# Kernel optimization log

Hardware: AMD Instinct MI355X
Metric: run time of the kernel (lower is better)

Reference implementation:

```python
import jax, jax.numpy as jnp
import numpy as np

D_MODEL = 1024
NUM_HEAD = 16
D_K = D_MODEL // NUM_HEAD


def setup_inputs() -> dict:
    key = jax.random.key(0)
    ks = jax.random.split(key, 11)
    B, S = 2, 2048
    s = 1.0 / np.sqrt(D_MODEL)
    return {
        "q": jax.random.normal(ks[0], (B, S, D_MODEL), jnp.float32),
        "k": jax.random.normal(ks[1], (B, S, D_MODEL), jnp.float32),
        "v": jax.random.normal(ks[2], (B, S, D_MODEL), jnp.float32),
        "Wq": jax.random.normal(ks[3], (D_MODEL, D_MODEL), jnp.float32) * s,
        "bq": jnp.zeros((D_MODEL,), jnp.float32),
        "Wk": jax.random.normal(ks[4], (D_MODEL, D_MODEL), jnp.float32) * s,
        "bk": jnp.zeros((D_MODEL,), jnp.float32),
        "Wv": jax.random.normal(ks[5], (D_MODEL, D_MODEL), jnp.float32) * s,
        "bv": jnp.zeros((D_MODEL,), jnp.float32),
        "Wo": jax.random.normal(ks[6], (D_MODEL, D_MODEL), jnp.float32) * s,
        "bo": jnp.zeros((D_MODEL,), jnp.float32),
    }


def _split_head(x, B):
    # [B, S, d_model] -> [B, H, S, d_k]
    S = x.shape[1]
    return x.reshape(B, S, NUM_HEAD, D_K).transpose(0, 2, 1, 3)


def reference(q, k, v, Wq, bq, Wk, bk, Wv, bv, Wo, bo):
    B = q.shape[0]
    qh = _split_head(q @ Wq + bq, B)  # [B,H,Sq,dk]
    kh = _split_head(k @ Wk + bk, B)  # [B,H,Sk,dk]
    vh = _split_head(v @ Wv + bv, B)  # [B,H,Sk,dk]
    scores = jnp.einsum("bhqd,bhkd->bhqk", qh, kh) / jnp.sqrt(
        jnp.asarray(D_K, qh.dtype)
    )
    attn = jax.nn.softmax(scores, axis=-1)
    out = jnp.einsum("bhqk,bhkd->bhqd", attn, vh)  # [B,H,Sq,dk]
    out = out.transpose(0, 2, 1, 3).reshape(B, -1, D_MODEL)
    return jax.nn.relu(out @ Wo + bo)
```

## Files before the change

### kernel.cpp

```cpp
#include <hip/hip_runtime.h>
#include <math.h>

#define SEQ 2048
#define NHD 16

typedef float f32x4 __attribute__((ext_vector_type(4), may_alias));
typedef _Float16 h16x8 __attribute__((ext_vector_type(8), may_alias));
typedef _Float16 h16x4 __attribute__((ext_vector_type(4), may_alias));

__device__ __forceinline__ void gl_lds16(const void* g, void* l) {
  __builtin_amdgcn_global_load_lds(
      (const __attribute__((address_space(1))) unsigned int*)g,
      (__attribute__((address_space(3))) unsigned int*)l, 16, 0, 0);
}

struct PrepArgs {
  const float* W[4];
  _Float16* T[4];
  const float* X[3];
  _Float16* H[3];
};

__global__ __launch_bounds__(256) void prep_k(PrepArgs a) {
  __shared__ float tile[64][65];
  const int blk = blockIdx.x;
  const int t = threadIdx.x;
  if (blk < 1024) {
    const int widx = blk >> 8, tl = blk & 255;
    const int nb = (tl & 15) * 64, kb = (tl >> 4) * 64;
    const float* __restrict__ W = a.W[widx];
    _Float16* __restrict__ T = a.T[widx];
    const int c = t & 63, r0 = t >> 6;
#pragma unroll
    for (int i = 0; i < 16; ++i) {
      const int r = i * 4 + r0;
      tile[r][c] = W[(size_t)(kb + r) * 1024 + nb + c];
    }
    __syncthreads();
#pragma unroll
    for (int i = 0; i < 16; ++i) {
      const int n = i * 4 + r0;
      T[(size_t)(nb + n) * 1024 + kb + c] = (_Float16)tile[c][n];
    }
  } else {
    const int b2 = blk - 1024;
    const int z = b2 >> 11, bx = b2 & 2047;
    const float* __restrict__ X = a.X[z];
    _Float16* __restrict__ H = a.H[z];
    const size_t i = ((size_t)bx * 256 + t) * 8;
    const f32x4 f0 = *(const f32x4*)(X + i);
    const f32x4 f1 = *(const f32x4*)(X + i + 4);
    const float fs[8] = {f0.x, f0.y, f0.z, f0.w, f1.x, f1.y, f1.z, f1.w};
    h16x8 o;
#pragma unroll
    for (int j = 0; j < 8; ++j) o[j] = (_Float16)fs[j];
    *(h16x8*)(H + i) = o;
  }
}

struct QKVArgs {
  const _Float16* A[3];
  const _Float16* Bt[3];
  const float* bias[3];
  _Float16* C[3];
};

__global__ __launch_bounds__(512, 2) void gemm_qkv_k(QKVArgs a) {
  __shared__ __align__(16) char smem[131072];
  const int dblk = blockIdx.x;
  const int z = dblk >> 6;
  const int rb = dblk & 63;
  const int m0 = (rb >> 2) * 256;
  const int n0 = (rb & 3) * 256;
  const _Float16* __restrict__ A = a.A[z];
  const _Float16* __restrict__ Bt = a.Bt[z];
  const float* __restrict__ bias = a.bias[z];
  _Float16* __restrict__ C = a.C[z];

  const int t = threadIdx.x;
  const int l = t & 63, w = t >> 6;
  const int quad = l >> 4, l15 = l & 15;
  const int wm = w >> 2, wn = w & 3;

  const int srow = t >> 3;
  const int sslot = (t & 7) ^ (srow & 7);
  size_t goffA[4], goffB[4];
#pragma unroll
  for (int j = 0; j < 4; ++j) {
    goffA[j] = (size_t)(m0 + j * 64 + srow) * 1024 + sslot * 8;
    goffB[j] = (size_t)(n0 + j * 64 + srow) * 1024 + sslot * 8;
  }

  auto stage = [&](int buf, int kt) {
    const int k0 = kt * 64;
    char* base = smem + buf * 65536;
#pragma unroll
    for (int j = 0; j < 4; ++j) {
      gl_lds16(A + goffA[j] + k0, base + j * 8192 + w * 1024);
      gl_lds16(Bt + goffB[j] + k0, base + 32768 + j * 8192 + w * 1024);
    }
  };

  const f32x4 z4 = {0.f, 0.f, 0.f, 0.f};
  f32x4 acc[8][4];
#pragma unroll
  for (int i = 0; i < 8; ++i)
#pragma unroll
    for (int j = 0; j < 4; ++j) acc[i][j] = z4;

  const int xr = l15 & 7;

  stage(0, 0);
  for (int kt = 0; kt < 16; ++kt) {
    const int cur = kt & 1;
    if (kt < 15) {
      stage(cur ^ 1, kt + 1);
      asm volatile("s_waitcnt vmcnt(8)" ::: "memory");
    } else {
      asm volatile("s_waitcnt vmcnt(0)" ::: "memory");
    }
    __builtin_amdgcn_sched_barrier(0);
    __builtin_amdgcn_s_barrier();

    const char* base = smem + cur * 65536;
    h16x8 bf[4][2];
#pragma unroll
    for (int nj = 0; nj < 4; ++nj) {
      const int rowB = wn * 64 + nj * 16 + l15;
#pragma unroll
      for (int h = 0; h < 2; ++h) {
        const int sl = (h * 4 + quad) ^ xr;
        bf[nj][h] = *(const h16x8*)(base + 32768 + rowB * 128 + sl * 16);
      }
    }
#pragma unroll
    for (int mi = 0; mi < 8; ++mi) {
      const int rowA = wm * 128 + mi * 16 + l15;
      const h16x8 af0 = *(const h16x8*)(base + rowA * 128 + ((quad ^ xr) * 16));
      const h16x8 af1 = *(const h16x8*)(base + rowA * 128 + (((4 + quad) ^ xr) * 16));
#pragma unroll
      for (int nj = 0; nj < 4; ++nj) {
        acc[mi][nj] = __builtin_amdgcn_mfma_f32_16x16x32_f16(af0, bf[nj][0], acc[mi][nj], 0, 0, 0);
        acc[mi][nj] = __builtin_amdgcn_mfma_f32_16x16x32_f16(af1, bf[nj][1], acc[mi][nj], 0, 0, 0);
      }
    }
    __builtin_amdgcn_sched_barrier(0);
    __builtin_amdgcn_s_barrier();
  }

  if (z < 2) {
#pragma unroll
    for (int mi = 0; mi < 8; ++mi)
#pragma unroll
      for (int nj = 0; nj < 4; ++nj) {
        const int col = n0 + wn * 64 + nj * 16 + l15;
        const float bv = bias[col];
#pragma unroll
        for (int r = 0; r < 4; ++r) {
          const int row = m0 + wm * 128 + mi * 16 + quad * 4 + r;
          const int b = row >> 11, s = row & 2047;
          const int h = col >> 6, d = col & 63;
          C[((size_t)(b * NHD + h) * SEQ + s) * 64 + d] = (_Float16)(acc[mi][nj][r] + bv);
        }
      }
  } else {
    _Float16* sh = (_Float16*)smem;
#pragma unroll
    for (int mi = 0; mi < 8; ++mi)
#pragma unroll
      for (int nj = 0; nj < 4; ++nj) {
        const int col = wn * 64 + nj * 16 + l15;
        const float bv = bias[n0 + col];
#pragma unroll
        for (int r = 0; r < 4; ++r) {
          const int row = wm * 128 + mi * 16 + quad * 4 + r;
          sh[row * 256 + col] = (_Float16)(acc[mi][nj][r] + bv);
        }
      }
    __syncthreads();
    const int dr = t >> 1;
    const int half = t & 1;
    const int hh = dr >> 6, d = dr & 63;
    const int b = m0 >> 11, sbase = m0 & 2047;
    const int colL = hh * 64 + d;
    const size_t gbase =
        ((size_t)((b * NHD + (n0 >> 6) + hh) * 64 + d)) * SEQ + sbase + half * 128;
#pragma unroll
    for (int m8 = 0; m8 < 16; ++m8) {
      const int qq = half * 128 + m8 * 8;
      h16x8 ov;
#pragma unroll
      for (int j = 0; j < 8; ++j) {
        const int q = qq + j;
        const int g = q >> 6, p = q & 63;
        const int c = (p >> 2) + ((p & 3) << 4);
        ov[j] = sh[(g * 64 + c) * 256 + colL];
      }
      *(h16x8*)(C + gbase + m8 * 8) = ov;
    }
  }
}

__global__ __launch_bounds__(256) void gemm_o_k(
    const _Float16* __restrict__ Op0, const _Float16* __restrict__ Op1,
    const float* __restrict__ Lp, const _Float16* __restrict__ Bt,
    const float* __restrict__ bias, float* __restrict__ Cf) {
  __shared__ char smem[40960];
  float* inv_lds = (float*)(smem + 32768);
  const int rb = blockIdx.x;
  const int n0 = ((rb >> 3) & 7) * 128;
  const int m0 = ((((rb >> 6) << 3) | (rb & 7))) * 128;
  const int t = threadIdx.x;
  const int l = t & 63, w = t >> 6;
  const int quad = l >> 4, l15 = l & 15;
  const int wm = w >> 1, wn = w & 1;
  const int arow0 = t >> 2, aq = t & 3;

#pragma unroll
  for (int e = t; e < 2048; e += 256) {
    const int rl = e >> 4, hh = e & 15;
    const int m = m0 + rl;
    const int b = m >> 11, s = m & 2047;
    const size_t li = (size_t)(b * NHD + hh) * 2048 + s;
    inv_lds[e] = 1.f / (Lp[li] + Lp[65536 + li]);
  }
  __syncthreads();

  auto stageB = [&](int buf, int k0) {
#pragma unroll
    for (int it = 0; it < 2; ++it) {
      const int c = it * 4 + w;
      const int rr = c * 16 + l15;
      gl_lds16(Bt + (size_t)(n0 + rr) * 1024 + k0 + quad * 8,
               smem + buf * 8192 + c * 1024);
    }
  };
  auto loadA = [&](int k0, h16x8 (&r0)[2], h16x8 (&r1)[2]) {
#pragma unroll
    for (int it = 0; it < 2; ++it) {
      const size_t off = (size_t)(m0 + it * 64 + arow0) * 1024 + k0 + aq * 8;
      r0[it] = *(const h16x8*)(Op0 + off);
      r1[it] = *(const h16x8*)(Op1 + off);
    }
  };
  auto writeA = [&](int buf, int k0, const h16x8 (&r0)[2], const h16x8 (&r1)[2]) {
    const int head = k0 >> 6;
    h16x8* alds = (h16x8*)(smem + 16384 + buf * 8192);
#pragma unroll
    for (int it = 0; it < 2; ++it) {
      const int row = it * 64 + arow0;
      const int slot = (row >> 4) * 64 + aq * 16 + ((row & 15) ^ (aq * 2));
      const float inv = inv_lds[row * 16 + head];
      h16x8 hv;
#pragma unroll
      for (int j = 0; j < 8; ++j)
        hv[j] = (_Float16)(((float)r0[it][j] + (float)r1[it][j]) * inv);
      alds[slot] = hv;
    }
  };

  const f32x4 z4 = {0.f, 0.f, 0.f, 0.f};
  f32x4 acc[4][4];
#pragma unroll
  for (int i = 0; i < 4; ++i)
#pragma unroll
    for (int j = 0; j < 4; ++j) acc[i][j] = z4;

  h16x8 a0r[2], a1r[2];
  loadA(0, a0r, a1r);
  stageB(0, 0);
  writeA(0, 0, a0r, a1r);
  __syncthreads();
  int cur = 0;
  for (int k0 = 0; k0 < 1024; k0 += 32) {
    const int nk = k0 + 32;
    if (nk < 1024) {
      loadA(nk, a0r, a1r);
      stageB(cur ^ 1, nk);
    }
    const h16x8* blds = (const h16x8*)(smem + cur * 8192);
    const h16x8* alds = (const h16x8*)(smem + 16384 + cur * 8192);
    h16x8 af[4], bf[4];
#pragma unroll
    for (int i = 0; i < 4; ++i) {
      af[i] = alds[(wm * 4 + i) * 64 + quad * 16 + (l15 ^ (quad * 2))];
      bf[i] = blds[(wn * 4 + i) * 64 + l];
    }
#pragma unroll
    for (int i = 0; i < 4; ++i)
#pragma unroll
      for (int j = 0; j < 4; ++j)
        acc[i][j] = __builtin_amdgcn_mfma_f32_16x16x32_f16(af[i], bf[j], acc[i][j], 0, 0, 0);
    if (nk < 1024) writeA(cur ^ 1, nk, a0r, a1r);
    __syncthreads();
    cur ^= 1;
  }
#pragma unroll
  for (int i = 0; i < 4; ++i)
#pragma unroll
    for (int j = 0; j < 4; ++j) {
      const int col = n0 + wn * 64 + j * 16 + l15;
      const float bv = bias[col];
#pragma unroll
      for (int r = 0; r < 4; ++r) {
        const int row = m0 + wm * 64 + i * 16 + quad * 4 + r;
        Cf[(size_t)row * 1024 + col] = fmaxf(acc[i][j][r] + bv, 0.f);
      }
    }
}

__global__ __launch_bounds__(256, 4) void attn_k(
    const _Float16* __restrict__ Qf, const _Float16* __restrict__ Kf,
    const _Float16* __restrict__ Vtp,
    _Float16* __restrict__ Op0, _Float16* __restrict__ Op1,
    float* __restrict__ Lp) {
  __shared__ char smem[34816];
  h16x8* lds8 = (h16x8*)smem;
  const int dblk = blockIdx.x;
  const int comb = ((dblk >> 7) << 3) | (dblk & 7);
  const int q0 = ((dblk >> 3) & 15) * 128;
  const int bh = comb >> 1;
  const int kz = comb & 1;
  const int t = threadIdx.x;
  const int l = t & 63, w = t >> 6;
  const int quad = l >> 4, l15 = l & 15;
  const int b = bh >> 4, h = bh & 15;

  const _Float16* Kb = Kf + (size_t)bh * SEQ * 64;
  const _Float16* Vtb = Vtp + (size_t)bh * 64 * SEQ;

  h16x8 qf[2][2];
#pragma unroll
  for (int mi = 0; mi < 2; ++mi) {
    const size_t qb = ((size_t)bh * SEQ + q0 + w * 32 + mi * 16 + l15) * 64;
#pragma unroll
    for (int ks = 0; ks < 2; ++ks)
      qf[mi][ks] = *(const h16x8*)&Qf[qb + ks * 32 + quad * 8];
  }
  const f32x4 z4 = {0.f, 0.f, 0.f, 0.f};
  f32x4 oacc[2][4], lacc[2];
#pragma unroll
  for (int mi = 0; mi < 2; ++mi) {
    lacc[mi] = z4;
#pragma unroll
    for (int i = 0; i < 4; ++i) oacc[mi][i] = z4;
  }
  h16x8 ones;
#pragma unroll
  for (int j = 0; j < 8; ++j) ones[j] = (_Float16)1.0f;

  const int kbeg = kz * 1024;
  for (int k0 = kbeg; k0 < kbeg + 1024; k0 += 64) {
#pragma unroll
    for (int it = 0; it < 2; ++it) {
      const int c = it * 4 + w;
      const int kd = (c >> 1) * 16 + l15;
      const int off2 = (c & 1) * 32 + quad * 8;
      gl_lds16(Kb + (size_t)(k0 + kd) * 64 + off2, smem + c * 1024);
      gl_lds16(Vtb + (size_t)kd * SEQ + k0 + off2, smem + 8192 + c * 1024);
    }
    __syncthreads();

    {
      h16x8 kfr[4][2];
#pragma unroll
      for (int nt = 0; nt < 4; ++nt)
#pragma unroll
        for (int ks = 0; ks < 2; ++ks) kfr[nt][ks] = lds8[(nt * 2 + ks) * 64 + l];

#pragma unroll
      for (int mi = 0; mi < 2; ++mi) {
        f32x4 sacc[4];
        __builtin_amdgcn_s_setprio(1);
#pragma unroll
        for (int nt = 0; nt < 4; ++nt) {
          f32x4 s = z4;
          s = __builtin_amdgcn_mfma_f32_16x16x32_f16(qf[mi][0], kfr[nt][0], s, 0, 0, 0);
          s = __builtin_amdgcn_mfma_f32_16x16x32_f16(qf[mi][1], kfr[nt][1], s, 0, 0, 0);
          sacc[nt] = s;
        }
        __builtin_amdgcn_s_setprio(0);
        char* pb = smem + 16384 + (w * 2 + mi) * 2304;
#pragma unroll
        for (int r = 0; r < 4; ++r) {
          h16x4 pk;
#pragma unroll
          for (int nt = 0; nt < 4; ++nt)
            pk[nt] = (_Float16)__expf(sacc[nt][r] * 0.125f);
          *(h16x4*)(pb + (quad * 4 + r) * 144 + l15 * 8) = pk;
        }
      }
    }
    __asm__ __volatile__("" ::: "memory");

    {
      h16x8 vfr[4][2];
#pragma unroll
      for (int nt = 0; nt < 4; ++nt)
#pragma unroll
        for (int ks = 0; ks < 2; ++ks) vfr[nt][ks] = lds8[512 + (nt * 2 + ks) * 64 + l];

      __builtin_amdgcn_s_setprio(1);
#pragma unroll
      for (int mi = 0; mi < 2; ++mi) {
        char* pb = smem + 16384 + (w * 2 + mi) * 2304;
        const h16x8 pf0 = *(const h16x8*)(pb + l15 * 144 + quad * 16);
        const h16x8 pf1 = *(const h16x8*)(pb + l15 * 144 + 64 + quad * 16);
        lacc[mi] = __builtin_amdgcn_mfma_f32_16x16x32_f16(pf0, ones, lacc[mi], 0, 0, 0);
        lacc[mi] = __builtin_amdgcn_mfma_f32_16x16x32_f16(pf1, ones, lacc[mi], 0, 0, 0);
#pragma unroll
        for (int nt = 0; nt < 4; ++nt) {
          oacc[mi][nt] = __builtin_amdgcn_mfma_f32_16x16x32_f16(pf0, vfr[nt][0], oacc[mi][nt], 0, 0, 0);
          oacc[mi][nt] = __builtin_amdgcn_mfma_f32_16x16x32_f16(pf1, vfr[nt][1], oacc[mi][nt], 0, 0, 0);
        }
      }
      __builtin_amdgcn_s_setprio(0);
    }
    __syncthreads();
  }

  _Float16* __restrict__ Op = kz ? Op1 : Op0;
#pragma unroll
  for (int mi = 0; mi < 2; ++mi)
#pragma unroll
    for (int nt = 0; nt < 4; ++nt)
#pragma unroll
      for (int r = 0; r < 4; ++r) {
        const size_t tok = (size_t)b * SEQ + q0 + w * 32 + mi * 16 + quad * 4 + r;
        Op[tok * 1024 + h * 64 + nt * 16 + l15] = (_Float16)oacc[mi][nt][r];
      }
  if (l15 == 0) {
#pragma unroll
    for (int mi = 0; mi < 2; ++mi)
#pragma unroll
      for (int r = 0; r < 4; ++r) {
        const int row = q0 + w * 32 + mi * 16 + quad * 4 + r;
        Lp[(size_t)kz * 65536 + bh * 2048 + row] = lacc[mi][r];
      }
  }
}

extern "C" void kernel_launch(void* const* d_in, const int* in_sizes, int n_in,
                              void* d_out, int out_size, void* d_ws, size_t ws_size,
                              hipStream_t stream) {
  const float* q = (const float*)d_in[0];
  const float* k = (const float*)d_in[1];
  const float* v = (const float*)d_in[2];
  const float* Wq = (const float*)d_in[3];
  const float* bq = (const float*)d_in[4];
  const float* Wk = (const float*)d_in[5];
  const float* bk = (const float*)d_in[6];
  const float* Wv = (const float*)d_in[7];
  const float* bv = (const float*)d_in[8];
  const float* Wo = (const float*)d_in[9];
  const float* bo = (const float*)d_in[10];

  char* W8 = (char*)d_ws;
  const size_t MB = 1024 * 1024;
  auto F = [&](size_t off) { return (_Float16*)(W8 + off); };
  _Float16* wt[4] = {F(0), F(2 * MB), F(4 * MB), F(6 * MB)};
  _Float16* qf = F(8 * MB);
  _Float16* kf = F(16 * MB);
  _Float16* vf = F(24 * MB);
  _Float16* Qf = F(32 * MB);
  _Float16* Kf = F(40 * MB);
  _Float16* Vt = F(56 * MB);
  _Float16* Op0 = F(8 * MB);
  _Float16* Op1 = F(16 * MB);
  float* Lp = (float*)(W8 + 64 * MB);

  const dim3 blk(256);

  PrepArgs pa;
  pa.W[0] = Wq; pa.W[1] = Wk; pa.W[2] = Wv; pa.W[3] = Wo;
  pa.T[0] = wt[0]; pa.T[1] = wt[1]; pa.T[2] = wt[2]; pa.T[3] = wt[3];
  pa.X[0] = q; pa.X[1] = k; pa.X[2] = v;
  pa.H[0] = qf; pa.H[1] = kf; pa.H[2] = vf;
  prep_k<<<dim3(7168), blk, 0, stream>>>(pa);

  QKVArgs qa;
  qa.A[0] = qf; qa.A[1] = kf; qa.A[2] = vf;
  qa.Bt[0] = wt[0]; qa.Bt[1] = wt[1]; qa.Bt[2] = wt[2];
  qa.bias[0] = bq; qa.bias[1] = bk; qa.bias[2] = bv;
  qa.C[0] = Qf; qa.C[1] = Kf; qa.C[2] = Vt;
  gemm_qkv_k<<<dim3(192), dim3(512), 0, stream>>>(qa);

  attn_k<<<dim3(1024), blk, 0, stream>>>(Qf, Kf, Vt, Op0, Op1, Lp);
  gemm_o_k<<<dim3(256), blk, 0, stream>>>(Op0, Op1, Lp, wt[3], bo, (float*)d_out);
}
```

Measured before the change: 240.0 us.

## Keep attention probabilities in registers via transposed QK^T MFMA and permuted V layout

Computes S^T by swapping MFMA operands (K as A, Q as B) so the exp'd scores land in registers in the layout the PV MFMA consumes. This removes the LDS round-trip for P, and the attention kernel's shared memory shrinks to K/V tiles only. The V-transpose prep kernel permutes the sequence index to match the new register layout. Q is also prescaled by 1/sqrt(dk) in fp16 once, which drops a multiply per score but adds a small rounding risk. The lower LDS use may allow more occupancy, though register pressure rises because K and V fragments are now held together.

```diff
diff --git a/kernel.cpp b/kernel.cpp
--- a/kernel.cpp
+++ b/kernel.cpp
@@ -193,7 +193,8 @@
       for (int j = 0; j < 8; ++j) {
         const int q = qq + j;
         const int g = q >> 6, p = q & 63;
-        const int c = (p >> 2) + ((p & 3) << 4);
+        const int c = (((p >> 5) << 1) | ((p >> 2) & 1)) * 16 +
+                      (((p >> 3) & 3) << 2) + (p & 3);
         ov[j] = sh[(g * 64 + c) * 256 + colL];
       }
       *(h16x8*)(C + gbase + m8 * 8) = ov;
@@ -314,7 +315,7 @@
     const _Float16* __restrict__ Vtp,
     _Float16* __restrict__ Op0, _Float16* __restrict__ Op1,
     float* __restrict__ Lp) {
-  __shared__ char smem[34816];
+  __shared__ __align__(16) char smem[16384];
   h16x8* lds8 = (h16x8*)smem;
   const int dblk = blockIdx.x;
   const int comb = ((dblk >> 7) << 3) | (dblk & 7);
@@ -337,6 +338,12 @@
     for (int ks = 0; ks < 2; ++ks)
       qf[mi][ks] = *(const h16x8*)&Qf[qb + ks * 32 + quad * 8];
   }
+  const _Float16 qs = (_Float16)0.125f;
+#pragma unroll
+  for (int mi = 0; mi < 2; ++mi)
+#pragma unroll
+    for (int ks = 0; ks < 2; ++ks) qf[mi][ks] = qf[mi][ks] * qs;
+
   const f32x4 z4 = {0.f, 0.f, 0.f, 0.f};
   f32x4 oacc[2][4], lacc[2];
 #pragma unroll
@@ -361,58 +368,42 @@
     }
     __syncthreads();
 
-    {
-      h16x8 kfr[4][2];
-#pragma unroll
-      for (int nt = 0; nt < 4; ++nt)
-#pragma unroll
-        for (int ks = 0; ks < 2; ++ks) kfr[nt][ks] = lds8[(nt * 2 + ks) * 64 + l];
-
-#pragma unroll
-      for (int mi = 0; mi < 2; ++mi) {
-        f32x4 sacc[4];
-        __builtin_amdgcn_s_setprio(1);
-#pragma unroll
-        for (int nt = 0; nt < 4; ++nt) {
-          f32x4 s = z4;
-          s = __builtin_amdgcn_mfma_f32_16x16x32_f16(qf[mi][0], kfr[nt][0], s, 0, 0, 0);
-          s = __builtin_amdgcn_mfma_f32_16x16x32_f16(qf[mi][1], kfr[nt][1], s, 0, 0, 0);
-          sacc[nt] = s;
-        }
-        __builtin_amdgcn_s_setprio(0);
-        char* pb = smem + 16384 + (w * 2 + mi) * 2304;
-#pragma unroll
-        for (int r = 0; r < 4; ++r) {
-          h16x4 pk;
-#pragma unroll
-          for (int nt = 0; nt < 4; ++nt)
-            pk[nt] = (_Float16)__expf(sacc[nt][r] * 0.125f);
-          *(h16x4*)(pb + (quad * 4 + r) * 144 + l15 * 8) = pk;
-        }
-      }
-    }
-    __asm__ __volatile__("" ::: "memory");
-
-    {
-      h16x8 vfr[4][2];
-#pragma unroll
-      for (int nt = 0; nt < 4; ++nt)
-#pragma unroll
-        for (int ks = 0; ks < 2; ++ks) vfr[nt][ks] = lds8[512 + (nt * 2 + ks) * 64 + l];
-
+    h16x8 kfr[4][2], vfr[4][2];
+#pragma unroll
+    for (int nt = 0; nt < 4; ++nt)
+#pragma unroll
+      for (int ks = 0; ks < 2; ++ks) {
+        kfr[nt][ks] = lds8[(nt * 2 + ks) * 64 + l];
+        vfr[nt][ks] = lds8[512 + (nt * 2 + ks) * 64 + l];
+      }
+
+#pragma unroll
+    for (int mi = 0; mi < 2; ++mi) {
+      f32x4 sacc[4];
       __builtin_amdgcn_s_setprio(1);
 #pragma unroll
-      for (int mi = 0; mi < 2; ++mi) {
-        char* pb = smem + 16384 + (w * 2 + mi) * 2304;
-        const h16x8 pf0 = *(const h16x8*)(pb + l15 * 144 + quad * 16);
-        const h16x8 pf1 = *(const h16x8*)(pb + l15 * 144 + 64 + quad * 16);
-        lacc[mi] = __builtin_amdgcn_mfma_f32_16x16x32_f16(pf0, ones, lacc[mi], 0, 0, 0);
-        lacc[mi] = __builtin_amdgcn_mfma_f32_16x16x32_f16(pf1, ones, lacc[mi], 0, 0, 0);
-#pragma unroll
-        for (int nt = 0; nt < 4; ++nt) {
-          oacc[mi][nt] = __builtin_amdgcn_mfma_f32_16x16x32_f16(pf0, vfr[nt][0], oacc[mi][nt], 0, 0, 0);
-          oacc[mi][nt] = __builtin_amdgcn_mfma_f32_16x16x32_f16(pf1, vfr[nt][1], oacc[mi][nt], 0, 0, 0);
-        }
+      for (int nt = 0; nt < 4; ++nt) {
+        f32x4 s = z4;
+        s = __builtin_amdgcn_mfma_f32_16x16x32_f16(kfr[nt][0], qf[mi][0], s, 0, 0, 0);
+        s = __builtin_amdgcn_mfma_f32_16x16x32_f16(kfr[nt][1], qf[mi][1], s, 0, 0, 0);
+        sacc[nt] = s;
+      }
+      __builtin_amdgcn_s_setprio(0);
+      h16x8 pa0, pa1;
+#pragma unroll
+      for (int r = 0; r < 4; ++r) {
+        pa0[r]     = (_Float16)__expf(sacc[0][r]);
+        pa0[4 + r] = (_Float16)__expf(sacc[1][r]);
+        pa1[r]     = (_Float16)__expf(sacc[2][r]);
+        pa1[4 + r] = (_Float16)__expf(sacc[3][r]);
+      }
+      __builtin_amdgcn_s_setprio(1);
+      lacc[mi] = __builtin_amdgcn_mfma_f32_16x16x32_f16(pa0, ones, lacc[mi], 0, 0, 0);
+      lacc[mi] = __builtin_amdgcn_mfma_f32_16x16x32_f16(pa1, ones, lacc[mi], 0, 0, 0);
+#pragma unroll
+      for (int nt = 0; nt < 4; ++nt) {
+        oacc[mi][nt] = __builtin_amdgcn_mfma_f32_16x16x32_f16(pa0, vfr[nt][0], oacc[mi][nt], 0, 0, 0);
+        oacc[mi][nt] = __builtin_amdgcn_mfma_f32_16x16x32_f16(pa1, vfr[nt][1], oacc[mi][nt], 0, 0, 0);
       }
       __builtin_amdgcn_s_setprio(0);
     }
```

Measured after the change: 327.1 us. +36.3%, slower.
